# Kernel tuning notes

Measured on AMD Instinct MI355X. Metric: run time of the kernel, lower is better.

## Reference

```python
import jax, jax.numpy as jnp
import numpy as np

B, C, D, H = 2, 1024, 1024, 16
DH = D // H
EPS = 1e-8


def setup_inputs() -> dict:
    key = jax.random.key(0)
    ks = jax.random.split(key, 12)
    s = 0.02
    return {
        "x": jax.random.normal(ks[0], (B, C, D), dtype=jnp.float32),
        "rms_w": jnp.ones((C, D), dtype=jnp.float32),
        "rms_b": jnp.zeros((C, D), dtype=jnp.float32),
        "Wqkv": jax.random.normal(ks[1], (3 * D, D), dtype=jnp.float32) * s,
        "Wout": jax.random.normal(ks[2], (D, D), dtype=jnp.float32) * s,
        "bout": jnp.zeros((D,), dtype=jnp.float32),
        "Wf": jax.random.normal(ks[3], (D, D), dtype=jnp.float32) * s,
        "bf": jnp.zeros((D,), dtype=jnp.float32),
        "Ww": jax.random.normal(ks[4], (D, D), dtype=jnp.float32) * s,
        "bw": jnp.zeros((D,), dtype=jnp.float32),
        "Wv": jax.random.normal(ks[5], (D, D), dtype=jnp.float32) * s,
        "bv": jnp.zeros((D,), dtype=jnp.float32),
        "beta": jnp.ones((1,), dtype=jnp.float32),
    }


def _rope_cos_sin(C, dh):
    # faithful to source: theta = 10000 ** (-2*(i-1)/dh), i in [0, dh//2)
    i = jnp.arange(dh // 2, dtype=jnp.float32)
    theta = 10000.0 ** (-2.0 * (i - 1.0) / dh)            # [dh//2]
    ang = jnp.arange(C, dtype=jnp.float32)[:, None] * theta  # [C, dh//2]
    return jnp.cos(ang), jnp.sin(ang)


def _rotate(t, cos, sin):
    # equivalent to einsum('bhci,cij->bhcj', t, R) with the source R
    ev, od = t[..., 0::2], t[..., 1::2]          # [B,H,C,dh//2]
    out_ev = ev * cos + od * sin
    out_od = -ev * sin + od * cos
    return jnp.stack([out_ev, out_od], axis=-1).reshape(t.shape)


def _rmsnorm(x, w, b):
    rms = jnp.sqrt(jnp.mean(x * x, axis=-1, keepdims=True) + EPS)
    return w * (x / rms) + b


def _attention(x, Wqkv, Wout, bout):
    qkv = x @ Wqkv.T                               # [B,C,3D]
    q, k, v = jnp.split(qkv, 3, axis=-1)
    def heads(t):
        return t.reshape(B, C, H, DH).transpose(0, 2, 1, 3)  # [B,H,C,dh]
    q, k, v = heads(q), heads(k), heads(v)
    cos, sin = _rope_cos_sin(C, DH)
    qr = _rotate(q, cos, sin)
    kr = _rotate(k, cos, sin)
    scale = 1.0 / jnp.sqrt(jnp.float32(DH))
    num = jnp.exp(jnp.einsum('bhid,bhjd->bhij', qr, kr) * scale)
    den = jnp.sum(jnp.exp(jnp.einsum('bhid,bhjd->bhij', q, k) * scale),
                  axis=-1, keepdims=True)
    attn = num / den
    mask = jnp.tril(jnp.ones((C, C), dtype=bool))
    attn = jnp.where(mask[None, None], attn, 0.0)
    y = attn @ v                                   # [B,H,C,dh]
    y = y.transpose(0, 2, 1, 3).reshape(B, C, D)
    return y @ Wout.T + bout


def _ffn(x, Wf, bf, Ww, bw, Wv, bv, beta):
    h = x @ Wf.T + bf
    wx = h @ Ww.T + bw
    swish = wx * jax.nn.sigmoid(beta * wx)
    return swish * (h @ Wv.T + bv)


def reference(x, rms_w, rms_b, Wqkv, Wout, bout, Wf, bf, Ww, bw, Wv, bv, beta):
    # dropout p is identity in eval mode
    x = _rmsnorm(x, rms_w, rms_b)
    x = x + _attention(x, Wqkv, Wout, bout)
    x = _rmsnorm(x, rms_w, rms_b)   # same shared RMSNorm module applied twice
    x = x + _ffn(x, Wf, bf, Ww, bw, Wv, bv, beta)
    return x
```

## Files before the change

kernel.cpp:

```cpp
#include <hip/hip_runtime.h>
#include <math.h>

#define B_ 2
#define C_ 1024
#define D_ 1024
#define H_ 16
#define DH_ 64
#define EPSF 1e-8f
#define BK 128

typedef __bf16 bf16;
typedef __attribute__((ext_vector_type(4))) __bf16 bf16x4;
typedef __attribute__((ext_vector_type(8))) __bf16 bf16x8;
typedef __attribute__((ext_vector_type(4))) float f32x4;

__device__ inline f32x4 mfma16(bf16x8 a, bf16x8 b, f32x4 c) {
  return __builtin_amdgcn_mfma_f32_16x16x32_bf16(a, b, c, 0, 0, 0);
}

__device__ inline void async16(const bf16* g, bf16* l) {
  __builtin_amdgcn_global_load_lds((const __attribute__((address_space(1))) void*)g,
                                   (__attribute__((address_space(3))) void*)l, 16, 0, 0);
}

__device__ inline float rope_theta(float i) {
  return exp2f(-13.287712379549449f * (2.0f * (i - 1.0f) * (1.0f / 64.0f)));
}

__global__ __launch_bounds__(256) void cvt_rms_kernel(const float* __restrict__ wqkv,
                                                      const float* __restrict__ wout,
                                                      const float* __restrict__ wf,
                                                      const float* __restrict__ www,
                                                      const float* __restrict__ wv,
                                                      bf16* __restrict__ wdst,
                                                      const float* __restrict__ x,
                                                      const float* __restrict__ rw,
                                                      const float* __restrict__ rb,
                                                      bf16* __restrict__ xout) {
  __shared__ float red[4];
  int t = threadIdx.x;
  if (blockIdx.x < 7 * 1024) {
    int seg = blockIdx.x >> 10;
    int local = (blockIdx.x & 1023) * 1024 + t * 4;
    const float* src = seg < 3 ? wqkv + (size_t)seg * (D_ * D_)
                     : seg == 3 ? wout : seg == 4 ? wf : seg == 5 ? www : wv;
    float4 v = *(const float4*)(src + local);
    bf16x4 o;
    o[0] = (bf16)v.x; o[1] = (bf16)v.y; o[2] = (bf16)v.z; o[3] = (bf16)v.w;
    *(bf16x4*)(wdst + (size_t)seg * (D_ * D_) + local) = o;
    return;
  }
  int row = blockIdx.x - 7 * 1024;
  int c = row & (C_ - 1);
  float4 xv = *(const float4*)(x + (size_t)row * D_ + t * 4);
  float ss = xv.x * xv.x + xv.y * xv.y + xv.z * xv.z + xv.w * xv.w;
#pragma unroll
  for (int m = 1; m < 64; m <<= 1) ss += __shfl_xor(ss, m, 64);
  if ((t & 63) == 0) red[t >> 6] = ss;
  __syncthreads();
  float tot = red[0] + red[1] + red[2] + red[3];
  float inv = rsqrtf(tot * (1.0f / D_) + EPSF);
  float4 wv4 = *(const float4*)(rw + (size_t)c * D_ + t * 4);
  float4 bv4 = *(const float4*)(rb + (size_t)c * D_ + t * 4);
  bf16x4 ov;
  ov[0] = (bf16)(wv4.x * (xv.x * inv) + bv4.x);
  ov[1] = (bf16)(wv4.y * (xv.y * inv) + bv4.y);
  ov[2] = (bf16)(wv4.z * (xv.z * inv) + bv4.z);
  ov[3] = (bf16)(wv4.w * (xv.w * inv) + bv4.w);
  *(bf16x4*)(xout + (size_t)row * D_ + t * 4) = ov;
}

__global__ __launch_bounds__(256) void rmsnorm_bf16_kernel(const bf16* __restrict__ x,
                                                           const float* __restrict__ w,
                                                           const float* __restrict__ b,
                                                           bf16* __restrict__ out) {
  int row = blockIdx.x;
  int c = row & (C_ - 1);
  int t = threadIdx.x;
  bf16x4 xv = *(const bf16x4*)(x + (size_t)row * D_ + t * 4);
  float f0 = (float)xv[0], f1 = (float)xv[1], f2 = (float)xv[2], f3 = (float)xv[3];
  float ss = f0 * f0 + f1 * f1 + f2 * f2 + f3 * f3;
#pragma unroll
  for (int m = 1; m < 64; m <<= 1) ss += __shfl_xor(ss, m, 64);
  __shared__ float red[4];
  if ((t & 63) == 0) red[t >> 6] = ss;
  __syncthreads();
  float tot = red[0] + red[1] + red[2] + red[3];
  float inv = rsqrtf(tot * (1.0f / D_) + EPSF);
  float4 wv = *(const float4*)(w + (size_t)c * D_ + t * 4);
  float4 bv = *(const float4*)(b + (size_t)c * D_ + t * 4);
  bf16x4 ov;
  ov[0] = (bf16)(wv.x * (f0 * inv) + bv.x);
  ov[1] = (bf16)(wv.y * (f1 * inv) + bv.y);
  ov[2] = (bf16)(wv.z * (f2 * inv) + bv.z);
  ov[3] = (bf16)(wv.w * (f3 * inv) + bv.w);
  *(bf16x4*)(out + (size_t)row * D_ + t * 4) = ov;
}

template <int BMt, int BNt>
__global__ __launch_bounds__(256) void gemm_lds(const bf16* __restrict__ A,
                                                const bf16* __restrict__ W,
                                                const float* __restrict__ bias,
                                                const bf16* __restrict__ R,
                                                bf16* __restrict__ Cout,
                                                int M, int N, int K) {
  constexpr int MT = BMt / 32;
  constexpr int NT = BNt / 32;
  __shared__ bf16 sa[BMt * BK];
  __shared__ bf16 sb[BNt * BK];
  int t = threadIdx.x, l = t & 63, w = t >> 6;
  int m0 = blockIdx.y * BMt;
  int n0 = blockIdx.x * BNt;
  int wm = (w >> 1) * (BMt / 2), wn = (w & 1) * (BNt / 2);
  int lm = l & 15, lq = l >> 4;
  int swz = lm & 7;
  f32x4 acc[MT][NT] = {};

  for (int k0 = 0; k0 < K; k0 += BK) {
    __syncthreads();
#pragma unroll
    for (int p = 0; p < BMt / 16; ++p) {
      int lin = p * 256 + t;
      int r = lin >> 4, cc = (lin & 15) ^ (r & 7);
      async16(A + (size_t)(m0 + r) * K + k0 + cc * 8, sa + lin * 8);
    }
#pragma unroll
    for (int p = 0; p < BNt / 16; ++p) {
      int lin = p * 256 + t;
      int r = lin >> 4, cc = (lin & 15) ^ (r & 7);
      async16(W + (size_t)(n0 + r) * K + k0 + cc * 8, sb + lin * 8);
    }
    __syncthreads();
#pragma unroll
    for (int hh = 0; hh < 4; ++hh) {
      bf16x8 af[MT], bfr[NT];
#pragma unroll
      for (int mt = 0; mt < MT; ++mt)
        af[mt] = *(const bf16x8*)(sa + (wm + mt * 16 + lm) * BK +
                                  ((((hh << 2) | lq) ^ swz) << 3));
#pragma unroll
      for (int nt = 0; nt < NT; ++nt)
        bfr[nt] = *(const bf16x8*)(sb + (wn + nt * 16 + lm) * BK +
                                   ((((hh << 2) | lq) ^ swz) << 3));
#pragma unroll
      for (int mt = 0; mt < MT; ++mt)
#pragma unroll
        for (int nt = 0; nt < NT; ++nt)
          acc[mt][nt] = mfma16(af[mt], bfr[nt], acc[mt][nt]);
    }
  }
#pragma unroll
  for (int mt = 0; mt < MT; ++mt)
#pragma unroll
    for (int nt = 0; nt < NT; ++nt) {
      int col = n0 + wn + nt * 16 + lm;
      float bb = bias ? bias[col] : 0.0f;
#pragma unroll
      for (int r = 0; r < 4; ++r) {
        int row = m0 + wm + mt * 16 + lq * 4 + r;
        float v = acc[mt][nt][r] + bb;
        if (R) v += (float)R[(size_t)row * N + col];
        Cout[(size_t)row * N + col] = (bf16)v;
      }
    }
}

__global__ __launch_bounds__(256) void gemm_qkv_kernel(const bf16* __restrict__ A,
                                                       const bf16* __restrict__ W,
                                                       bf16* __restrict__ qkv,
                                                       bf16* __restrict__ vt) {
  constexpr int BMt = 128, BNt = 64, MT = 4, NT = 2;
  const int N = 3 * D_, K = D_;
  __shared__ bf16 sa[BMt * BK];
  __shared__ bf16 sb[BNt * BK];
  int t = threadIdx.x, l = t & 63, w = t >> 6;
  int m0 = blockIdx.y * BMt;
  int n0 = blockIdx.x * BNt;
  int wm = (w >> 1) * 64, wn = (w & 1) * 32;
  int lm = l & 15, lq = l >> 4;
  int swz = lm & 7;
  f32x4 acc[MT][NT] = {};

  for (int k0 = 0; k0 < K; k0 += BK) {
    __syncthreads();
#pragma unroll
    for (int p = 0; p < 8; ++p) {
      int lin = p * 256 + t;
      int r = lin >> 4, cc = (lin & 15) ^ (r & 7);
      async16(A + (size_t)(m0 + r) * K + k0 + cc * 8, sa + lin * 8);
    }
#pragma unroll
    for (int p = 0; p < 4; ++p) {
      int lin = p * 256 + t;
      int r = lin >> 4, cc = (lin & 15) ^ (r & 7);
      async16(W + (size_t)(n0 + r) * K + k0 + cc * 8, sb + lin * 8);
    }
    __syncthreads();
#pragma unroll
    for (int hh = 0; hh < 4; ++hh) {
      bf16x8 af[MT], bfr[NT];
#pragma unroll
      for (int mt = 0; mt < MT; ++mt)
        af[mt] = *(const bf16x8*)(sa + (wm + mt * 16 + lm) * BK +
                                  ((((hh << 2) | lq) ^ swz) << 3));
#pragma unroll
      for (int nt = 0; nt < NT; ++nt)
        bfr[nt] = *(const bf16x8*)(sb + (wn + nt * 16 + lm) * BK +
                                   ((((hh << 2) | lq) ^ swz) << 3));
#pragma unroll
      for (int mt = 0; mt < MT; ++mt)
#pragma unroll
        for (int nt = 0; nt < NT; ++nt)
          acc[mt][nt] = mfma16(af[mt], bfr[nt], acc[mt][nt]);
    }
  }
  if (n0 < 2 * D_) {
#pragma unroll
    for (int mt = 0; mt < MT; ++mt)
#pragma unroll
      for (int nt = 0; nt < NT; ++nt) {
        int col = n0 + wn + nt * 16 + lm;
#pragma unroll
        for (int r = 0; r < 4; ++r) {
          int row = m0 + wm + mt * 16 + lq * 4 + r;
          qkv[(size_t)row * N + col] = (bf16)acc[mt][nt][r];
        }
      }
  } else {
    __syncthreads();
    bf16* tv = sa;
#pragma unroll
    for (int mt = 0; mt < MT; ++mt)
#pragma unroll
      for (int nt = 0; nt < NT; ++nt) {
        int dh = wn + nt * 16 + lm;
#pragma unroll
        for (int r = 0; r < 4; ++r)
          tv[dh * 136 + wm + mt * 16 + lq * 4 + r] = (bf16)acc[mt][nt][r];
      }
    __syncthreads();
    int h = (n0 - 2 * D_) >> 6;
    int bb = m0 >> 10;
    int mloc = m0 & 1023;
    size_t vbase = (size_t)((bb * H_ + h) * DH_) * C_;
#pragma unroll
    for (int p = 0; p < 4; ++p) {
      int lin = p * 256 + t;
      int dh = lin >> 4;
      int mm = (lin & 15) * 8;
      *(int4*)(vt + vbase + (size_t)dh * C_ + mloc + mm) = *(int4*)(tv + dh * 136 + mm);
    }
  }
}

__global__ __launch_bounds__(256) void gemm_ffn_kernel(const bf16* __restrict__ A,
                                                       const bf16* __restrict__ Ww,
                                                       const bf16* __restrict__ Wv,
                                                       const float* __restrict__ bw,
                                                       const float* __restrict__ bv,
                                                       const bf16* __restrict__ x3,
                                                       const float* __restrict__ beta_p,
                                                       float* __restrict__ out) {
  __shared__ bf16 sa[64 * BK];
  __shared__ bf16 sb1[64 * BK];
  __shared__ bf16 sb2[64 * BK];
  int t = threadIdx.x, l = t & 63, w = t >> 6;
  int m0 = blockIdx.y * 64, n0 = blockIdx.x * 64;
  int wm = (w >> 1) * 32, wn = (w & 1) * 32;
  int lm = l & 15, lq = l >> 4;
  int swz = lm & 7;
  float beta = beta_p[0];
  f32x4 acc1[2][2] = {}, acc2[2][2] = {};

  for (int k0 = 0; k0 < D_; k0 += BK) {
    __syncthreads();
#pragma unroll
    for (int p = 0; p < 4; ++p) {
      int lin = p * 256 + t;
      int r = lin >> 4, cc = (lin & 15) ^ (r & 7);
      async16(A + (size_t)(m0 + r) * D_ + k0 + cc * 8, sa + lin * 8);
      async16(Ww + (size_t)(n0 + r) * D_ + k0 + cc * 8, sb1 + lin * 8);
      async16(Wv + (size_t)(n0 + r) * D_ + k0 + cc * 8, sb2 + lin * 8);
    }
    __syncthreads();
#pragma unroll
    for (int hh = 0; hh < 4; ++hh) {
      int co = (((hh << 2) | lq) ^ swz) << 3;
      bf16x8 af[2], b1f[2], b2f[2];
#pragma unroll
      for (int mt = 0; mt < 2; ++mt)
        af[mt] = *(const bf16x8*)(sa + (wm + mt * 16 + lm) * BK + co);
#pragma unroll
      for (int nt = 0; nt < 2; ++nt) {
        b1f[nt] = *(const bf16x8*)(sb1 + (wn + nt * 16 + lm) * BK + co);
        b2f[nt] = *(const bf16x8*)(sb2 + (wn + nt * 16 + lm) * BK + co);
      }
#pragma unroll
      for (int mt = 0; mt < 2; ++mt)
#pragma unroll
        for (int nt = 0; nt < 2; ++nt) {
          acc1[mt][nt] = mfma16(af[mt], b1f[nt], acc1[mt][nt]);
          acc2[mt][nt] = mfma16(af[mt], b2f[nt], acc2[mt][nt]);
        }
    }
  }
#pragma unroll
  for (int mt = 0; mt < 2; ++mt)
#pragma unroll
    for (int nt = 0; nt < 2; ++nt) {
      int col = n0 + wn + nt * 16 + lm;
      float bbw = bw[col], bbv = bv[col];
#pragma unroll
      for (int r = 0; r < 4; ++r) {
        int row = m0 + wm + mt * 16 + lq * 4 + r;
        float z = acc1[mt][nt][r] + bbw;
        float g = acc2[mt][nt][r] + bbv;
        float sw_ = z / (1.0f + __expf(-beta * z));
        out[(size_t)row * D_ + col] = (float)x3[(size_t)row * D_ + col] + sw_ * g;
      }
    }
}

__global__ __launch_bounds__(256) void attn_kernel(const bf16* __restrict__ qkv,
                                                   const bf16* __restrict__ vt,
                                                   bf16* __restrict__ y) {
  __shared__ bf16 sk[64 * 72];
  __shared__ bf16 skr[64 * 72];
  __shared__ bf16 sv[64 * 72];
  __shared__ bf16 pl[4][16 * 72];
  int t = threadIdx.x, l = t & 63, w = t >> 6;
  int blk = blockIdx.x;
  int idx = blk & 255;
  int it = (blk < 256) ? (idx >> 5) : (15 - (idx >> 5));
  int r5 = idx & 31;
  int b = r5 >> 4;
  int h = r5 & 15;
  int i_base = it * 64 + w * 16;
  int lm = l & 15, lq = l >> 4;
  const float scale = 0.125f;

  size_t hq = (size_t)h * DH_;
  size_t qrow = (size_t)(b * C_ + i_base + lm) * (3 * D_) + hq;
  bf16x8 qp[2], qrf[2];
  float cq = (float)(i_base + lm);
#pragma unroll
  for (int kk = 0; kk < 2; ++kk) {
    qp[kk] = *(const bf16x8*)(qkv + qrow + kk * 32 + lq * 8);
#pragma unroll
    for (int j = 0; j < 4; ++j) {
      float ip = (float)(kk * 16 + lq * 4 + j);
      float ang = cq * rope_theta(ip);
      float sv_, cv_;
      __sincosf(ang, &sv_, &cv_);
      float qe = (float)qp[kk][2 * j], qo = (float)qp[kk][2 * j + 1];
      qrf[kk][2 * j] = (bf16)(qe * cv_ + qo * sv_);
      qrf[kk][2 * j + 1] = (bf16)(qo * cv_ - qe * sv_);
    }
  }

  float den[4] = {0.f, 0.f, 0.f, 0.f};
  f32x4 yacc[4] = {};
  int i_max = i_base + 15;
  size_t kbase = (size_t)(b * C_) * (3 * D_) + D_ + hq;
  size_t vtbase = (size_t)((b * H_ + h) * DH_) * C_;
  int sr = t >> 3;
  int sc = (t & 7) * 8;
  float th0 = rope_theta((float)((sc >> 1) + 0));
  float th1 = rope_theta((float)((sc >> 1) + 1));
  float th2 = rope_theta((float)((sc >> 1) + 2));
  float th3 = rope_theta((float)((sc >> 1) + 3));

  int4 pk0, pk1, pv0, pv1, rk0, rk1;
#define FETCH_TILE(J0)                                                          \
  pk0 = *(const int4*)(qkv + kbase + (size_t)((J0) + sr) * (3 * D_) + sc);      \
  pk1 = *(const int4*)(qkv + kbase + (size_t)((J0) + 32 + sr) * (3 * D_) + sc); \
  pv0 = *(const int4*)(vt + vtbase + (size_t)sr * C_ + (J0) + sc);              \
  pv1 = *(const int4*)(vt + vtbase + (size_t)(32 + sr) * C_ + (J0) + sc);

#define ROTP(KV, RV, P)                                       \
  {                                                           \
    float e = (float)KV[2 * P], o = (float)KV[2 * P + 1];     \
    RV[2 * P] = (bf16)(e * c_ + o * s_);                      \
    RV[2 * P + 1] = (bf16)(o * c_ - e * s_);                  \
  }
#define ROTATE(J0)                                            \
  {                                                           \
    bf16x8 k0 = *(bf16x8*)&pk0, k1 = *(bf16x8*)&pk1;          \
    bf16x8 r0, r1;                                            \
    float jA = (float)((J0) + sr), jB = (float)((J0) + 32 + sr); \
    float s_, c_;                                             \
    __sincosf(jA * th0, &s_, &c_); ROTP(k0, r0, 0)            \
    __sincosf(jA * th1, &s_, &c_); ROTP(k0, r0, 1)            \
    __sincosf(jA * th2, &s_, &c_); ROTP(k0, r0, 2)            \
    __sincosf(jA * th3, &s_, &c_); ROTP(k0, r0, 3)            \
    __sincosf(jB * th0, &s_, &c_); ROTP(k1, r1, 0)            \
    __sincosf(jB * th1, &s_, &c_); ROTP(k1, r1, 1)            \
    __sincosf(jB * th2, &s_, &c_); ROTP(k1, r1, 2)            \
    __sincosf(jB * th3, &s_, &c_); ROTP(k1, r1, 3)            \
    rk0 = *(int4*)&r0;                                        \
    rk1 = *(int4*)&r1;                                        \
  }

  FETCH_TILE(0)
  ROTATE(0)

  for (int j0 = 0; j0 < C_; j0 += 64) {
    __syncthreads();
    *(int4*)(sk + sr * 72 + sc) = pk0;
    *(int4*)(sk + (32 + sr) * 72 + sc) = pk1;
    *(int4*)(skr + sr * 72 + sc) = rk0;
    *(int4*)(skr + (32 + sr) * 72 + sc) = rk1;
    *(int4*)(sv + sr * 72 + sc) = pv0;
    *(int4*)(sv + (32 + sr) * 72 + sc) = pv1;
    __syncthreads();
    if (j0 + 64 < C_) {
      FETCH_TILE(j0 + 64)
    }
#pragma unroll
    for (int js = 0; js < 64; js += 16) {
      bf16x8 kf0 = *(const bf16x8*)(sk + (js + lm) * 72 + lq * 8);
      bf16x8 kf1 = *(const bf16x8*)(sk + (js + lm) * 72 + 32 + lq * 8);
      f32x4 s = {0.f, 0.f, 0.f, 0.f};
      s = mfma16(qp[0], kf0, s);
      s = mfma16(qp[1], kf1, s);
#pragma unroll
      for (int r = 0; r < 4; ++r) den[r] += __expf(s[r] * scale);
    }
    if (j0 <= i_max) {
#pragma unroll
      for (int js = 0; js < 64; js += 16) {
        bf16x8 kf0 = *(const bf16x8*)(skr + (js + lm) * 72 + lq * 8);
        bf16x8 kf1 = *(const bf16x8*)(skr + (js + lm) * 72 + 32 + lq * 8);
        f32x4 s = {0.f, 0.f, 0.f, 0.f};
        s = mfma16(qrf[0], kf0, s);
        s = mfma16(qrf[1], kf1, s);
#pragma unroll
        for (int r = 0; r < 4; ++r) {
          int jg = j0 + js + lm;
          int ig = i_base + lq * 4 + r;
          float p = (jg <= ig) ? __expf(s[r] * scale) : 0.0f;
          pl[w][(lq * 4 + r) * 72 + js + lm] = (bf16)p;
        }
      }
      __builtin_amdgcn_wave_barrier();
      bf16x8 pf0 = *(const bf16x8*)(pl[w] + lm * 72 + lq * 8);
      bf16x8 pf1 = *(const bf16x8*)(pl[w] + lm * 72 + 32 + lq * 8);
#pragma unroll
      for (int tt = 0; tt < 4; ++tt) {
        bf16x8 vf0 = *(const bf16x8*)(sv + (tt * 16 + lm) * 72 + lq * 8);
        bf16x8 vf1 = *(const bf16x8*)(sv + (tt * 16 + lm) * 72 + 32 + lq * 8);
        yacc[tt] = mfma16(pf0, vf0, mfma16(pf1, vf1, yacc[tt]));
      }
      __builtin_amdgcn_wave_barrier();
    }
    if (j0 + 64 < C_) {
      ROTATE(j0 + 64)
    }
  }
#undef FETCH_TILE
#undef ROTATE
#undef ROTP
  float inv[4];
#pragma unroll
  for (int r = 0; r < 4; ++r) {
    float d = den[r];
    d += __shfl_xor(d, 1, 64);
    d += __shfl_xor(d, 2, 64);
    d += __shfl_xor(d, 4, 64);
    d += __shfl_xor(d, 8, 64);
    inv[r] = 1.0f / d;
  }
#pragma unroll
  for (int tt = 0; tt < 4; ++tt)
#pragma unroll
    for (int r = 0; r < 4; ++r) {
      int ig = i_base + lq * 4 + r;
      y[(size_t)(b * C_ + ig) * D_ + hq + tt * 16 + lm] = (bf16)(yacc[tt][r] * inv[r]);
    }
}

extern "C" void kernel_launch(void* const* d_in, const int* in_sizes, int n_in,
                              void* d_out, int out_size, void* d_ws, size_t ws_size,
                              hipStream_t stream) {
  const float* x = (const float*)d_in[0];
  const float* rms_w = (const float*)d_in[1];
  const float* rms_b = (const float*)d_in[2];
  const float* Wqkv = (const float*)d_in[3];
  const float* Wout = (const float*)d_in[4];
  const float* bout = (const float*)d_in[5];
  const float* Wf = (const float*)d_in[6];
  const float* bfp = (const float*)d_in[7];
  const float* Ww = (const float*)d_in[8];
  const float* bw = (const float*)d_in[9];
  const float* Wv = (const float*)d_in[10];
  const float* bv = (const float*)d_in[11];
  const float* beta = (const float*)d_in[12];
  float* out = (float*)d_out;

  bf16* ws = (bf16*)d_ws;
  const size_t DD = (size_t)D_ * D_;
  const size_t MC = (size_t)B_ * C_;
  bf16* wb = ws;
  bf16* x1 = ws + 7 * DD;
  bf16* qkv = ws + 9 * DD;
  bf16* vt = ws + 15 * DD;
  bf16* x2 = ws + 17 * DD;
  bf16* x3 = ws + 19 * DD;
  bf16* hbuf = ws + 21 * DD;
  bf16* y = (bf16*)d_out;

  cvt_rms_kernel<<<7 * 1024 + MC, 256, 0, stream>>>(Wqkv, Wout, Wf, Ww, Wv, wb, x, rms_w,
                                                    rms_b, x1);
  gemm_qkv_kernel<<<dim3(3 * D_ / 64, MC / 128), 256, 0, stream>>>(x1, wb, qkv, vt);
  attn_kernel<<<B_ * H_ * 16, 256, 0, stream>>>(qkv, vt, y);
  gemm_lds<64, 64><<<dim3(D_ / 64, MC / 64), 256, 0, stream>>>(
      y, wb + 3 * DD, bout, x1, x2, MC, D_, D_);
  rmsnorm_bf16_kernel<<<MC, 256, 0, stream>>>(x2, rms_w, rms_b, x3);
  gemm_lds<64, 64><<<dim3(D_ / 64, MC / 64), 256, 0, stream>>>(
      x3, wb + 4 * DD, bfp, nullptr, hbuf, MC, D_, D_);
  gemm_ffn_kernel<<<dim3(D_ / 64, MC / 64), 256, 0, stream>>>(
      hbuf, wb + 5 * DD, wb + 6 * DD, bw, bv, x3, beta, out);
}
```

Before: 203.9 us.

## Double-buffer LDS tiles in GEMM kernels with async prefetch and vmcnt waits

Converts the generic, QKV and FFN GEMM kernels to double-buffered LDS. The next K-tile is issued via global_load_lds while the current tile is multiplied, with explicit s_waitcnt vmcnt and s_barrier replacing __syncthreads. The QKV and FFN kernels also drop BK from 128 to 64 so the doubled buffers fit in LDS and occupancy holds up. The hand-written vmcnt counts must match the number of outstanding loads per stage, and the smaller BK means more loop iterations and barriers.

```diff
diff --git a/kernel.cpp b/kernel.cpp
--- a/kernel.cpp
+++ b/kernel.cpp
@@ -7,7 +7,6 @@
 #define H_ 16
 #define DH_ 64
 #define EPSF 1e-8f
-#define BK 128
 
 typedef __bf16 bf16;
 typedef __attribute__((ext_vector_type(4))) __bf16 bf16x4;
@@ -22,6 +21,9 @@
   __builtin_amdgcn_global_load_lds((const __attribute__((address_space(1))) void*)g,
                                    (__attribute__((address_space(3))) void*)l, 16, 0, 0);
 }
+
+#define S_BARRIER() asm volatile("s_barrier" ::: "memory")
+#define S_VMCNT(N) asm volatile("s_waitcnt vmcnt(" #N ")" ::: "memory")
 
 __device__ inline float rope_theta(float i) {
   return exp2f(-13.287712379549449f * (2.0f * (i - 1.0f) * (1.0f / 64.0f)));
@@ -104,10 +106,11 @@
                                                 const bf16* __restrict__ R,
                                                 bf16* __restrict__ Cout,
                                                 int M, int N, int K) {
+  constexpr int BK = 128;
   constexpr int MT = BMt / 32;
   constexpr int NT = BNt / 32;
-  __shared__ bf16 sa[BMt * BK];
-  __shared__ bf16 sb[BNt * BK];
+  __shared__ bf16 sa[2][BMt * BK];
+  __shared__ bf16 sb[2][BNt * BK];
   int t = threadIdx.x, l = t & 63, w = t >> 6;
   int m0 = blockIdx.y * BMt;
   int n0 = blockIdx.x * BNt;
@@ -116,31 +119,42 @@
   int swz = lm & 7;
   f32x4 acc[MT][NT] = {};
 
-  for (int k0 = 0; k0 < K; k0 += BK) {
-    __syncthreads();
+  auto stage = [&](int buf, int k0) {
 #pragma unroll
     for (int p = 0; p < BMt / 16; ++p) {
       int lin = p * 256 + t;
       int r = lin >> 4, cc = (lin & 15) ^ (r & 7);
-      async16(A + (size_t)(m0 + r) * K + k0 + cc * 8, sa + lin * 8);
+      async16(A + (size_t)(m0 + r) * K + k0 + cc * 8, &sa[buf][lin * 8]);
     }
 #pragma unroll
     for (int p = 0; p < BNt / 16; ++p) {
       int lin = p * 256 + t;
       int r = lin >> 4, cc = (lin & 15) ^ (r & 7);
-      async16(W + (size_t)(n0 + r) * K + k0 + cc * 8, sb + lin * 8);
-    }
-    __syncthreads();
+      async16(W + (size_t)(n0 + r) * K + k0 + cc * 8, &sb[buf][lin * 8]);
+    }
+  };
+
+  int NKi = K / BK;
+  stage(0, 0);
+  int cur = 0;
+  for (int i = 0; i < NKi; ++i) {
+    if (i + 1 < NKi) {
+      stage(cur ^ 1, (i + 1) * BK);
+      S_VMCNT(8);
+    } else {
+      S_VMCNT(0);
+    }
+    S_BARRIER();
 #pragma unroll
     for (int hh = 0; hh < 4; ++hh) {
       bf16x8 af[MT], bfr[NT];
 #pragma unroll
       for (int mt = 0; mt < MT; ++mt)
-        af[mt] = *(const bf16x8*)(sa + (wm + mt * 16 + lm) * BK +
+        af[mt] = *(const bf16x8*)(&sa[cur][0] + (wm + mt * 16 + lm) * BK +
                                   ((((hh << 2) | lq) ^ swz) << 3));
 #pragma unroll
       for (int nt = 0; nt < NT; ++nt)
-        bfr[nt] = *(const bf16x8*)(sb + (wn + nt * 16 + lm) * BK +
+        bfr[nt] = *(const bf16x8*)(&sb[cur][0] + (wn + nt * 16 + lm) * BK +
                                    ((((hh << 2) | lq) ^ swz) << 3));
 #pragma unroll
       for (int mt = 0; mt < MT; ++mt)
@@ -148,6 +162,8 @@
         for (int nt = 0; nt < NT; ++nt)
           acc[mt][nt] = mfma16(af[mt], bfr[nt], acc[mt][nt]);
     }
+    S_BARRIER();
+    cur ^= 1;
   }
 #pragma unroll
   for (int mt = 0; mt < MT; ++mt)
@@ -169,10 +185,11 @@
                                                        const bf16* __restrict__ W,
                                                        bf16* __restrict__ qkv,
                                                        bf16* __restrict__ vt) {
+  constexpr int BK = 64;
   constexpr int BMt = 128, BNt = 64, MT = 4, NT = 2;
   const int N = 3 * D_, K = D_;
-  __shared__ bf16 sa[BMt * BK];
-  __shared__ bf16 sb[BNt * BK];
+  __shared__ bf16 sa[2][BMt * BK];
+  __shared__ bf16 sb[2][BNt * BK];
   int t = threadIdx.x, l = t & 63, w = t >> 6;
   int m0 = blockIdx.y * BMt;
   int n0 = blockIdx.x * BNt;
@@ -181,38 +198,54 @@
   int swz = lm & 7;
   f32x4 acc[MT][NT] = {};
 
-  for (int k0 = 0; k0 < K; k0 += BK) {
-    __syncthreads();
-#pragma unroll
-    for (int p = 0; p < 8; ++p) {
-      int lin = p * 256 + t;
-      int r = lin >> 4, cc = (lin & 15) ^ (r & 7);
-      async16(A + (size_t)(m0 + r) * K + k0 + cc * 8, sa + lin * 8);
-    }
+  auto stage = [&](int buf, int k0) {
 #pragma unroll
     for (int p = 0; p < 4; ++p) {
       int lin = p * 256 + t;
-      int r = lin >> 4, cc = (lin & 15) ^ (r & 7);
-      async16(W + (size_t)(n0 + r) * K + k0 + cc * 8, sb + lin * 8);
-    }
-    __syncthreads();
-#pragma unroll
-    for (int hh = 0; hh < 4; ++hh) {
-      bf16x8 af[MT], bfr[NT];
-#pragma unroll
-      for (int mt = 0; mt < MT; ++mt)
-        af[mt] = *(const bf16x8*)(sa + (wm + mt * 16 + lm) * BK +
-                                  ((((hh << 2) | lq) ^ swz) << 3));
-#pragma unroll
-      for (int nt = 0; nt < NT; ++nt)
-        bfr[nt] = *(const bf16x8*)(sb + (wn + nt * 16 + lm) * BK +
-                                   ((((hh << 2) | lq) ^ swz) << 3));
-#pragma unroll
-      for (int mt = 0; mt < MT; ++mt)
-#pragma unroll
-        for (int nt = 0; nt < NT; ++nt)
-          acc[mt][nt] = mfma16(af[mt], bfr[nt], acc[mt][nt]);
-    }
+      int r = lin >> 3, cc = (lin & 7) ^ (r & 7);
+      async16(A + (size_t)(m0 + r) * K + k0 + cc * 8, &sa[buf][lin * 8]);
+    }
+#pragma unroll
+    for (int p = 0; p < 2; ++p) {
+      int lin = p * 256 + t;
+      int r = lin >> 3, cc = (lin & 7) ^ (r & 7);
+      async16(W + (size_t)(n0 + r) * K + k0 + cc * 8, &sb[buf][lin * 8]);
+    }
+  };
+
+  int NKi = K / BK;
+  stage(0, 0);
+  int cur = 0;
+  for (int i = 0; i < NKi; ++i) {
+    if (i + 1 < NKi) {
+      stage(cur ^ 1, (i + 1) * BK);
+      S_VMCNT(6);
+    } else {
+      S_VMCNT(0);
+    }
+    S_BARRIER();
+    bf16x8 af[MT][2], bfr[NT][2];
+#pragma unroll
+    for (int mt = 0; mt < MT; ++mt) {
+      const bf16* base = &sa[cur][0] + (wm + mt * 16 + lm) * BK;
+      af[mt][0] = *(const bf16x8*)(base + ((lq ^ swz) << 3));
+      af[mt][1] = *(const bf16x8*)(base + (((4 | lq) ^ swz) << 3));
+    }
+#pragma unroll
+    for (int nt = 0; nt < NT; ++nt) {
+      const bf16* base = &sb[cur][0] + (wn + nt * 16 + lm) * BK;
+      bfr[nt][0] = *(const bf16x8*)(base + ((lq ^ swz) << 3));
+      bfr[nt][1] = *(const bf16x8*)(base + (((4 | lq) ^ swz) << 3));
+    }
+#pragma unroll
+    for (int mt = 0; mt < MT; ++mt)
+#pragma unroll
+      for (int nt = 0; nt < NT; ++nt) {
+        acc[mt][nt] = mfma16(af[mt][0], bfr[nt][0], acc[mt][nt]);
+        acc[mt][nt] = mfma16(af[mt][1], bfr[nt][1], acc[mt][nt]);
+      }
+    S_BARRIER();
+    cur ^= 1;
   }
   if (n0 < 2 * D_) {
 #pragma unroll
@@ -227,8 +260,7 @@
         }
       }
   } else {
-    __syncthreads();
-    bf16* tv = sa;
+    bf16* tv = &sa[0][0];
 #pragma unroll
     for (int mt = 0; mt < MT; ++mt)
 #pragma unroll
@@ -261,9 +293,10 @@
                                                        const bf16* __restrict__ x3,
                                                        const float* __restrict__ beta_p,
                                                        float* __restrict__ out) {
-  __shared__ bf16 sa[64 * BK];
-  __shared__ bf16 sb1[64 * BK];
-  __shared__ bf16 sb2[64 * BK];
+  constexpr int BK = 64;
+  __shared__ bf16 sa[2][64 * BK];
+  __shared__ bf16 sb1[2][64 * BK];
+  __shared__ bf16 sb2[2][64 * BK];
   int t = threadIdx.x, l = t & 63, w = t >> 6;
   int m0 = blockIdx.y * 64, n0 = blockIdx.x * 64;
   int wm = (w >> 1) * 32, wn = (w & 1) * 32;
@@ -272,37 +305,55 @@
   float beta = beta_p[0];
   f32x4 acc1[2][2] = {}, acc2[2][2] = {};
 
-  for (int k0 = 0; k0 < D_; k0 += BK) {
-    __syncthreads();
-#pragma unroll
-    for (int p = 0; p < 4; ++p) {
+  auto stage = [&](int buf, int k0) {
+#pragma unroll
+    for (int p = 0; p < 2; ++p) {
       int lin = p * 256 + t;
-      int r = lin >> 4, cc = (lin & 15) ^ (r & 7);
-      async16(A + (size_t)(m0 + r) * D_ + k0 + cc * 8, sa + lin * 8);
-      async16(Ww + (size_t)(n0 + r) * D_ + k0 + cc * 8, sb1 + lin * 8);
-      async16(Wv + (size_t)(n0 + r) * D_ + k0 + cc * 8, sb2 + lin * 8);
-    }
-    __syncthreads();
-#pragma unroll
-    for (int hh = 0; hh < 4; ++hh) {
-      int co = (((hh << 2) | lq) ^ swz) << 3;
-      bf16x8 af[2], b1f[2], b2f[2];
-#pragma unroll
-      for (int mt = 0; mt < 2; ++mt)
-        af[mt] = *(const bf16x8*)(sa + (wm + mt * 16 + lm) * BK + co);
+      int r = lin >> 3, cc = (lin & 7) ^ (r & 7);
+      async16(A + (size_t)(m0 + r) * D_ + k0 + cc * 8, &sa[buf][lin * 8]);
+      async16(Ww + (size_t)(n0 + r) * D_ + k0 + cc * 8, &sb1[buf][lin * 8]);
+      async16(Wv + (size_t)(n0 + r) * D_ + k0 + cc * 8, &sb2[buf][lin * 8]);
+    }
+  };
+
+  int NKi = D_ / BK;
+  stage(0, 0);
+  int cur = 0;
+  for (int i = 0; i < NKi; ++i) {
+    if (i + 1 < NKi) {
+      stage(cur ^ 1, (i + 1) * BK);
+      S_VMCNT(6);
+    } else {
+      S_VMCNT(0);
+    }
+    S_BARRIER();
+    bf16x8 af[2][2], b1f[2][2], b2f[2][2];
+#pragma unroll
+    for (int mt = 0; mt < 2; ++mt) {
+      const bf16* base = &sa[cur][0] + (wm + mt * 16 + lm) * BK;
+      af[mt][0] = *(const bf16x8*)(base + ((lq ^ swz) << 3));
+      af[mt][1] = *(const bf16x8*)(base + (((4 | lq) ^ swz) << 3));
+    }
+#pragma unroll
+    for (int nt = 0; nt < 2; ++nt) {
+      const bf16* base1 = &sb1[cur][0] + (wn + nt * 16 + lm) * BK;
+      const bf16* base2 = &sb2[cur][0] + (wn + nt * 16 + lm) * BK;
+      b1f[nt][0] = *(const bf16x8*)(base1 + ((lq ^ swz) << 3));
+      b1f[nt][1] = *(const bf16x8*)(base1 + (((4 | lq) ^ swz) << 3));
+      b2f[nt][0] = *(const bf16x8*)(base2 + ((lq ^ swz) << 3));
+      b2f[nt][1] = *(const bf16x8*)(base2 + (((4 | lq) ^ swz) << 3));
+    }
+#pragma unroll
+    for (int mt = 0; mt < 2; ++mt)
 #pragma unroll
       for (int nt = 0; nt < 2; ++nt) {
-        b1f[nt] = *(const bf16x8*)(sb1 + (wn + nt * 16 + lm) * BK + co);
-        b2f[nt] = *(const bf16x8*)(sb2 + (wn + nt * 16 + lm) * BK + co);
-      }
-#pragma unroll
-      for (int mt = 0; mt < 2; ++mt)
-#pragma unroll
-        for (int nt = 0; nt < 2; ++nt) {
-          acc1[mt][nt] = mfma16(af[mt], b1f[nt], acc1[mt][nt]);
-          acc2[mt][nt] = mfma16(af[mt], b2f[nt], acc2[mt][nt]);
-        }
-    }
+        acc1[mt][nt] = mfma16(af[mt][0], b1f[nt][0], acc1[mt][nt]);
+        acc1[mt][nt] = mfma16(af[mt][1], b1f[nt][1], acc1[mt][nt]);
+        acc2[mt][nt] = mfma16(af[mt][0], b2f[nt][0], acc2[mt][nt]);
+        acc2[mt][nt] = mfma16(af[mt][1], b2f[nt][1], acc2[mt][nt]);
+      }
+    S_BARRIER();
+    cur ^= 1;
   }
 #pragma unroll
   for (int mt = 0; mt < 2; ++mt)
```

Measured after the change: 203.9 us. Within noise of the previous version (-0.0%).
